# Kernel tuning notes

Hardware: AMD Instinct MI355X
Metric: run time of the kernel (lower is better)

Reference implementation:

```python
import jax, jax.numpy as jnp
import numpy as np

N = 30000          # num nodes
E = 480000         # num edges (avg degree 16)
IN = 1024          # in_channels
OUT = 128          # out_channels
MAX_DEG = 48       # static cap on per-node in-degree (incl. self-loop); Poisson(16) max over 30k nodes << 48


def setup_inputs() -> dict:
    key = jax.random.key(0)
    k1, k2, k3 = jax.random.split(key, 3)
    x = jax.random.normal(k1, (N, IN), dtype=jnp.float32)
    edge_index = jax.random.randint(k2, (2, E), 0, N, dtype=jnp.int64)
    W = jax.random.normal(k3, (IN, OUT), dtype=jnp.float32) * (1.0 / np.sqrt(IN))
    b = jnp.zeros((OUT,), dtype=jnp.float32)
    return {"x": x, "edge_index": edge_index, "W": W, "b": b}


def _median_conv(x, edge_index, W, b):
    # linear transform first (as in the torch module)
    h = x @ W                                   # [N, OUT]
    n = x.shape[0]
    # add self-loops
    loop = jnp.arange(n, dtype=edge_index.dtype)
    row = jnp.concatenate([edge_index[0], loop])  # source nodes
    col = jnp.concatenate([edge_index[1], loop])  # destination nodes
    # sort edges by destination (jnp.argsort is stable)
    order = jnp.argsort(col)
    row_s = row[order]
    col_s = col[order]
    x_j = h[row_s]                              # [Etot, OUT] gathered neighbor features
    # per-destination degree and within-segment slot index
    ones = jnp.ones_like(col_s)
    deg = jax.ops.segment_sum(ones, col_s, num_segments=n)      # [N]
    start = jnp.cumsum(deg) - deg                                # segment start offsets
    slot = jnp.arange(col_s.shape[0], dtype=col_s.dtype) - start[col_s]
    # padded dense batch [N, MAX_DEG, OUT]; pads = +inf so they sort to the end
    dense = jnp.full((n, MAX_DEG, h.shape[1]), jnp.inf, dtype=h.dtype)
    dense = dense.at[col_s, slot].set(x_j)
    sdense = jnp.sort(dense, axis=1)
    # torch.median returns the LOWER median: sorted index (deg-1)//2
    med_idx = jnp.maximum(deg - 1, 0) // 2                       # [N]
    out = jnp.take_along_axis(sdense, med_idx[:, None, None], axis=1)[:, 0, :]
    # zero-degree nodes would yield +inf; self-loops guarantee deg>=1, but guard anyway
    out = jnp.where((deg > 0)[:, None], out, jnp.zeros_like(out))
    return out + b


def reference(x, edge_index, W, b):
    return _median_conv(x, edge_index, W, b)
```

## Files before the change

### kernel.cpp

```cpp
#include <hip/hip_runtime.h>
#include <hip/hip_bf16.h>

#define N_NODES 30000
#define N_EDGES 480000
#define IN_CH   1024
#define OUT_CH  128
#define MAX_DEG 48

#define BM 128
#define BK 64
#define NSTEP (IN_CH / BK)

typedef float   f32x4  __attribute__((ext_vector_type(4)));
typedef __bf16  bf16x8 __attribute__((ext_vector_type(8)));
typedef unsigned short ushort8 __attribute__((ext_vector_type(8)));

__device__ __forceinline__ unsigned short f2bf(float f) {
  unsigned int u = __builtin_bit_cast(unsigned int, f);
  u += 0x7fffu + ((u >> 16) & 1u);
  return (unsigned short)(u >> 16);
}

__device__ __forceinline__ void gload_lds16(const float* g, float* l) {
  __builtin_amdgcn_global_load_lds(
      (const __attribute__((address_space(1))) void*)g,
      (__attribute__((address_space(3))) void*)l, 16, 0, 0);
}

__global__ __launch_bounds__(256) void convert_W(const float* __restrict__ W,
                                                 unsigned short* __restrict__ Wt) {
  int idx = blockIdx.x * 256 + threadIdx.x;
  int n = idx >> 10;
  int k = idx & 1023;
  Wt[idx] = f2bf(W[k * OUT_CH + n]);
}

__global__ __launch_bounds__(256) void build_adj(const int* __restrict__ ei,
                                                 int* __restrict__ deg,
                                                 int* __restrict__ adj) {
  int i = blockIdx.x * blockDim.x + threadIdx.x;
  const int total = N_EDGES + N_NODES;
  if (i >= total) return;
  int src, dst;
  if (i < N_EDGES) { src = ei[i]; dst = ei[N_EDGES + i]; }
  else             { src = i - N_EDGES; dst = src; }
  int slot = atomicAdd(&deg[dst], 1);
  if (slot < MAX_DEG) adj[dst * MAX_DEG + slot] = src;
}

__global__ __launch_bounds__(256) void gemm_h(const float* __restrict__ x,
                                              const unsigned short* __restrict__ Wt,
                                              const float* __restrict__ bias,
                                              float* __restrict__ h) {
  __shared__ float smem[2 * BM * BK];
  const int tid  = threadIdx.x;
  const int wave = tid >> 6;
  const int lane = tid & 63;
  const int l16  = lane & 15;
  const int g4   = lane >> 4;
  const int m0   = blockIdx.x * BM;
  const int trow = tid >> 4;
  const int tcol = tid & 15;

  f32x4 acc[8][2];
#pragma unroll
  for (int rf = 0; rf < 8; ++rf)
#pragma unroll
    for (int cf = 0; cf < 2; ++cf) acc[rf][cf] = (f32x4){0.f, 0.f, 0.f, 0.f};

  auto stage = [&](int buf, int st) {
    const int k0 = st * BK;
#pragma unroll
    for (int r = 0; r < 8; ++r) {
      int row_t = r * 16 + trow;
      int row_g = m0 + row_t;
      if (row_g > N_NODES - 1) row_g = N_NODES - 1;
      int ksw = (tcol ^ (row_t & 7)) << 2;
      const float* src = x + (size_t)row_g * IN_CH + k0 + ksw;
      float* dst = smem + buf * (BM * BK) + row_t * BK + tcol * 4;
      gload_lds16(src, dst);
    }
  };

  auto compute = [&](int buf, int st) {
    const int k0 = st * BK;
    const char* sb = (const char*)(smem + buf * (BM * BK));
#pragma unroll
    for (int ks = 0; ks < 2; ++ks) {
      bf16x8 bfr[2];
#pragma unroll
      for (int cf = 0; cf < 2; ++cf) {
        int col = wave * 32 + cf * 16 + l16;
        ushort8 bu = *(const ushort8*)(Wt + (size_t)col * IN_CH + k0 + ks * 32 + g4 * 8);
        bfr[cf] = __builtin_bit_cast(bf16x8, bu);
      }
#pragma unroll
      for (int rf = 0; rf < 8; ++rf) {
        int row = rf * 16 + l16;
        int s   = (row & 7) << 4;
        int b0  = (row << 8) + ((ks * 32 + g4 * 8) << 2);
        f32x4 a0 = *(const f32x4*)(sb + ((b0) ^ s));
        f32x4 a1 = *(const f32x4*)(sb + ((b0 + 16) ^ s));
        ushort8 af;
        af[0] = f2bf(a0[0]); af[1] = f2bf(a0[1]); af[2] = f2bf(a0[2]); af[3] = f2bf(a0[3]);
        af[4] = f2bf(a1[0]); af[5] = f2bf(a1[1]); af[6] = f2bf(a1[2]); af[7] = f2bf(a1[3]);
        bf16x8 av = __builtin_bit_cast(bf16x8, af);
        acc[rf][0] = __builtin_amdgcn_mfma_f32_16x16x32_bf16(av, bfr[0], acc[rf][0], 0, 0, 0);
        acc[rf][1] = __builtin_amdgcn_mfma_f32_16x16x32_bf16(av, bfr[1], acc[rf][1], 0, 0, 0);
      }
    }
  };

  stage(0, 0);
  __syncthreads();
  int cur = 0;
  for (int st = 0; st < NSTEP - 1; ++st) {
    stage(cur ^ 1, st + 1);
    compute(cur, st);
    __syncthreads();
    cur ^= 1;
  }
  compute(cur, NSTEP - 1);

  const int crow0 = m0 + g4 * 4;
#pragma unroll
  for (int cf = 0; cf < 2; ++cf) {
    const int col = wave * 32 + cf * 16 + l16;
    const float bv = bias[col];
#pragma unroll
    for (int rf = 0; rf < 8; ++rf) {
#pragma unroll
      for (int i = 0; i < 4; ++i) {
        int r = crow0 + rf * 16 + i;
        if (r < N_NODES) h[(size_t)r * OUT_CH + col] = acc[rf][cf][i] + bv;
      }
    }
  }
}

template <int NS>
__device__ __forceinline__ void batcher_sort(float (&a)[NS]) {
#pragma unroll
  for (int p = 1; p < NS; p <<= 1) {
#pragma unroll
    for (int k = p; k >= 1; k >>= 1) {
#pragma unroll
      for (int j = k % p; j + k < NS; j += 2 * k) {
#pragma unroll
        for (int i = 0; i < k; ++i) {
          if (i + j + k < NS) {
            if ((i + j) / (2 * p) == (i + j + k) / (2 * p)) {
              float lo = fminf(a[i + j], a[i + j + k]);
              float hi = fmaxf(a[i + j], a[i + j + k]);
              a[i + j] = lo;
              a[i + j + k] = hi;
            }
          }
        }
      }
    }
  }
}

template <int NS>
__device__ __forceinline__ float med_n(const float* __restrict__ h,
                                       const int* nbrs, int d, int m, int ch) {
  float a[NS];
#pragma unroll
  for (int j = 0; j < NS; ++j) {
    if (j < d) a[j] = h[(size_t)nbrs[j] * OUT_CH + ch];
    else       a[j] = 1e30f;
  }
  batcher_sort<NS>(a);
  float med = a[0];
#pragma unroll
  for (int j = 1; j < NS; ++j) med = (j == m) ? a[j] : med;
  return med;
}

__global__ __launch_bounds__(128) void median_kernel(const float* __restrict__ h,
                                                     const int* __restrict__ adj,
                                                     const int* __restrict__ deg,
                                                     float* __restrict__ out) {
  __shared__ int nbrs[64];
  const int node = blockIdx.x;
  const int ch   = threadIdx.x;
  int d = deg[node];
  if (d > MAX_DEG) d = MAX_DEG;
  if (ch < 64) nbrs[ch] = (ch < d && ch < MAX_DEG) ? adj[node * MAX_DEG + ch] : 0;
  __syncthreads();
  const int m = (d - 1) >> 1;

  float med;
  if (d <= 8)       med = med_n<8>(h, nbrs, d, m, ch);
  else if (d <= 16) med = med_n<16>(h, nbrs, d, m, ch);
  else if (d <= 32) med = med_n<32>(h, nbrs, d, m, ch);
  else              med = med_n<64>(h, nbrs, d, m, ch);

  out[(size_t)node * OUT_CH + ch] = med;
}

extern "C" void kernel_launch(void* const* d_in, const int* in_sizes, int n_in,
                              void* d_out, int out_size, void* d_ws, size_t ws_size,
                              hipStream_t stream) {
  const float* x  = (const float*)d_in[0];
  const int*   ei = (const int*)d_in[1];
  const float* W  = (const float*)d_in[2];
  const float* b  = (const float*)d_in[3];
  float* out = (float*)d_out;

  char* ws = (char*)d_ws;
  float*          h   = (float*)ws;
  unsigned short* Wt  = (unsigned short*)(ws + 15360000);
  int*            deg = (int*)(ws + 15360000 + 262144);
  int*            adj = (int*)(ws + 15360000 + 262144 + 120000);

  hipMemsetAsync(deg, 0, N_NODES * sizeof(int), stream);
  convert_W<<<dim3(131072 / 256), dim3(256), 0, stream>>>(W, Wt);
  build_adj<<<dim3((N_EDGES + N_NODES + 255) / 256), dim3(256), 0, stream>>>(ei, deg, adj);
  gemm_h<<<dim3((N_NODES + BM - 1) / BM), dim3(256), 0, stream>>>(x, Wt, b, h);
  median_kernel<<<dim3(N_NODES), dim3(128), 0, stream>>>(h, adj, deg, out);
}
```

Baseline: 294.8 us.

## Stage W tile in LDS, halve GEMM row tile, use packed bf16 convert

The GEMM now loads the bf16 W tile into shared memory alongside the x tile using async global-to-LDS copies, instead of each wave reading W directly from global memory every k-step. The row tile shrinks from 128 to 64, which doubles the block count to improve occupancy across CUs, and the swizzle is changed to a 16-way XOR pattern. The fp32-to-bf16 conversion of A now uses the hardware v_cvt_pk_bf16_f32 instruction instead of manual rounding. The smaller tile lowers reuse of W per block, and the median kernel, which likely dominates runtime, is not changed.

```diff
diff --git a/kernel.cpp b/kernel.cpp
--- a/kernel.cpp
+++ b/kernel.cpp
@@ -7,13 +7,14 @@
 #define OUT_CH  128
 #define MAX_DEG 48
 
-#define BM 128
+#define BM 64
 #define BK 64
 #define NSTEP (IN_CH / BK)
 
 typedef float   f32x4  __attribute__((ext_vector_type(4)));
 typedef __bf16  bf16x8 __attribute__((ext_vector_type(8)));
 typedef unsigned short ushort8 __attribute__((ext_vector_type(8)));
+typedef unsigned int   uint4v  __attribute__((ext_vector_type(4)));
 
 __device__ __forceinline__ unsigned short f2bf(float f) {
   unsigned int u = __builtin_bit_cast(unsigned int, f);
@@ -21,7 +22,13 @@
   return (unsigned short)(u >> 16);
 }
 
-__device__ __forceinline__ void gload_lds16(const float* g, float* l) {
+__device__ __forceinline__ unsigned int cvt_pk(float lo, float hi) {
+  unsigned int r;
+  asm("v_cvt_pk_bf16_f32 %0, %1, %2" : "=v"(r) : "v"(lo), "v"(hi));
+  return r;
+}
+
+__device__ __forceinline__ void gload_lds16(const void* g, void* l) {
   __builtin_amdgcn_global_load_lds(
       (const __attribute__((address_space(1))) void*)g,
       (__attribute__((address_space(3))) void*)l, 16, 0, 0);
@@ -52,59 +59,65 @@
                                               const unsigned short* __restrict__ Wt,
                                               const float* __restrict__ bias,
                                               float* __restrict__ h) {
-  __shared__ float smem[2 * BM * BK];
+  __shared__ char smem[2 * 32768];
   const int tid  = threadIdx.x;
-  const int wave = tid >> 6;
+  const int wv   = tid >> 6;
   const int lane = tid & 63;
   const int l16  = lane & 15;
   const int g4   = lane >> 4;
   const int m0   = blockIdx.x * BM;
-  const int trow = tid >> 4;
-  const int tcol = tid & 15;
-
-  f32x4 acc[8][2];
-#pragma unroll
-  for (int rf = 0; rf < 8; ++rf)
+
+  f32x4 acc[4][2];
+#pragma unroll
+  for (int rf = 0; rf < 4; ++rf)
 #pragma unroll
     for (int cf = 0; cf < 2; ++cf) acc[rf][cf] = (f32x4){0.f, 0.f, 0.f, 0.f};
 
   auto stage = [&](int buf, int st) {
     const int k0 = st * BK;
-#pragma unroll
-    for (int r = 0; r < 8; ++r) {
-      int row_t = r * 16 + trow;
-      int row_g = m0 + row_t;
-      if (row_g > N_NODES - 1) row_g = N_NODES - 1;
-      int ksw = (tcol ^ (row_t & 7)) << 2;
-      const float* src = x + (size_t)row_g * IN_CH + k0 + ksw;
-      float* dst = smem + buf * (BM * BK) + row_t * BK + tcol * 4;
-      gload_lds16(src, dst);
+    char* sA = smem + buf * 32768;
+    char* sB = sA + 16384;
+#pragma unroll
+    for (int j = 0; j < 4; ++j) {
+      const int blk = wv * 4 + j;
+      const int rowA = blk * 4 + (lane >> 4);
+      int rg = m0 + rowA;
+      if (rg > N_NODES - 1) rg = N_NODES - 1;
+      const float* srcA = x + (size_t)rg * IN_CH + k0
+                        + (((lane & 15) ^ (rowA & 15)) << 2);
+      gload_lds16(srcA, sA + blk * 1024 + lane * 16);
+      const int c = blk * 8 + (lane >> 3);
+      const unsigned short* srcB = Wt + (size_t)c * IN_CH + k0
+                                 + (((lane & 7) ^ (c & 7)) << 3);
+      gload_lds16(srcB, sB + blk * 1024 + lane * 16);
     }
   };
 
-  auto compute = [&](int buf, int st) {
-    const int k0 = st * BK;
-    const char* sb = (const char*)(smem + buf * (BM * BK));
+  auto compute = [&](int buf) {
+    const char* sA = smem + buf * 32768;
+    const char* sB = sA + 16384;
 #pragma unroll
     for (int ks = 0; ks < 2; ++ks) {
       bf16x8 bfr[2];
 #pragma unroll
       for (int cf = 0; cf < 2; ++cf) {
-        int col = wave * 32 + cf * 16 + l16;
-        ushort8 bu = *(const ushort8*)(Wt + (size_t)col * IN_CH + k0 + ks * 32 + g4 * 8);
-        bfr[cf] = __builtin_bit_cast(bf16x8, bu);
-      }
-#pragma unroll
-      for (int rf = 0; rf < 8; ++rf) {
-        int row = rf * 16 + l16;
-        int s   = (row & 7) << 4;
-        int b0  = (row << 8) + ((ks * 32 + g4 * 8) << 2);
-        f32x4 a0 = *(const f32x4*)(sb + ((b0) ^ s));
-        f32x4 a1 = *(const f32x4*)(sb + ((b0 + 16) ^ s));
-        ushort8 af;
-        af[0] = f2bf(a0[0]); af[1] = f2bf(a0[1]); af[2] = f2bf(a0[2]); af[3] = f2bf(a0[3]);
-        af[4] = f2bf(a1[0]); af[5] = f2bf(a1[1]); af[6] = f2bf(a1[2]); af[7] = f2bf(a1[3]);
-        bf16x8 av = __builtin_bit_cast(bf16x8, af);
+        const int c = wv * 32 + cf * 16 + l16;
+        const int slot = (ks * 4 + g4) ^ (c & 7);
+        bfr[cf] = *(const bf16x8*)(sB + c * 128 + slot * 16);
+      }
+#pragma unroll
+      for (int rf = 0; rf < 4; ++rf) {
+        const int row = rf * 16 + l16;
+        const int q0 = ((ks * 8 + g4 * 2) ^ (row & 15)) << 4;
+        const int q1 = ((ks * 8 + g4 * 2 + 1) ^ (row & 15)) << 4;
+        f32x4 a0 = *(const f32x4*)(sA + row * 256 + q0);
+        f32x4 a1 = *(const f32x4*)(sA + row * 256 + q1);
+        uint4v aw;
+        aw[0] = cvt_pk(a0[0], a0[1]);
+        aw[1] = cvt_pk(a0[2], a0[3]);
+        aw[2] = cvt_pk(a1[0], a1[1]);
+        aw[3] = cvt_pk(a1[2], a1[3]);
+        bf16x8 av = __builtin_bit_cast(bf16x8, aw);
         acc[rf][0] = __builtin_amdgcn_mfma_f32_16x16x32_bf16(av, bfr[0], acc[rf][0], 0, 0, 0);
         acc[rf][1] = __builtin_amdgcn_mfma_f32_16x16x32_bf16(av, bfr[1], acc[rf][1], 0, 0, 0);
       }
@@ -116,19 +129,19 @@
   int cur = 0;
   for (int st = 0; st < NSTEP - 1; ++st) {
     stage(cur ^ 1, st + 1);
-    compute(cur, st);
+    compute(cur);
     __syncthreads();
     cur ^= 1;
   }
-  compute(cur, NSTEP - 1);
+  compute(cur);
 
   const int crow0 = m0 + g4 * 4;
 #pragma unroll
   for (int cf = 0; cf < 2; ++cf) {
-    const int col = wave * 32 + cf * 16 + l16;
+    const int col = wv * 32 + cf * 16 + l16;
     const float bv = bias[col];
 #pragma unroll
-    for (int rf = 0; rf < 8; ++rf) {
+    for (int rf = 0; rf < 4; ++rf) {
 #pragma unroll
       for (int i = 0; i < 4; ++i) {
         int r = crow0 + rf * 16 + i;
```

After: 273.9 us. 1.08x faster.
